# Performance work log

Hardware: AMD Instinct MI355X
Metric: run time of the kernel (lower is better)

The kernel has to match this reference:

```python
import jax, jax.numpy as jnp
import numpy as np

B, S = 32, 128
E_NUM, SKILL, D_K, D_E, D_A = 4000, 256, 128, 128, 128
AT_NUM, IT_NUM = 1000, 1000
GAMMA = 0.03


def _lin(key, out_d, in_d):
    # xavier-normal style init
    w = jax.random.normal(key, (out_d, in_d), jnp.float32) * (2.0 / (in_d + out_d)) ** 0.5
    b = jnp.zeros((out_d,), jnp.float32)
    return w, b


def setup_inputs() -> dict:
    key = jax.random.key(0)
    ks = jax.random.split(key, 16)
    exercise_id = jax.random.randint(ks[0], (B, S), 0, E_NUM, jnp.int32)
    ans_time = jax.random.randint(ks[1], (B, S), 0, AT_NUM, jnp.int32)
    interval_time = jax.random.randint(ks[2], (B, S), 0, IT_NUM, jnp.int32)
    answer_value = jax.random.randint(ks[3], (B, S), 0, 2, jnp.int32)
    # enhanced q-matrix: binary with zeros replaced by gamma
    qmask = jax.random.bernoulli(ks[4], 0.1, (E_NUM, SKILL))
    q_matrix = jnp.where(qmask, 1.0, GAMMA).astype(jnp.float32)
    ex_table = jax.random.normal(ks[5], (E_NUM, D_E), jnp.float32)
    at_table = jax.random.normal(ks[6], (AT_NUM, D_K), jnp.float32)
    it_table = jax.random.normal(ks[7], (IT_NUM, D_K), jnp.float32)
    W1, b1 = _lin(ks[8], D_K, D_E + D_K + D_A)   # learning_embed_layer
    Wl, bl = _lin(ks[9], D_K, 4 * D_K)           # learning_layer
    Wg, bg = _lin(ks[10], D_K, 4 * D_K)          # learning_gate
    Wf, bf = _lin(ks[11], D_K, 3 * D_K)          # forgetting_gate
    Wp, bp = _lin(ks[12], D_K, 2 * D_K)          # predicting_layer
    # xavier-uniform initial knowledge state, shared across batch
    lim = (6.0 / (SKILL + D_K)) ** 0.5
    h0 = jax.random.uniform(ks[13], (SKILL, D_K), jnp.float32, -lim, lim)
    return {"exercise_id": exercise_id, "ans_time": ans_time,
            "interval_time": interval_time, "answer_value": answer_value,
            "q_matrix": q_matrix, "ex_table": ex_table, "at_table": at_table,
            "it_table": it_table, "W1": W1, "b1": b1, "Wl": Wl, "bl": bl,
            "Wg": Wg, "bg": bg, "Wf": Wf, "bf": bf, "Wp": Wp, "bp": bp, "h0": h0}


def _forward(exercise_id, ans_time, interval_time, answer_value, q_matrix,
             ex_table, at_table, it_table, W1, b1, Wl, bl, Wg, bg, Wf, bf,
             Wp, bp, h0):
    b, s = exercise_id.shape
    ex = ex_table[exercise_id]                       # (B,S,d_e)
    at = at_table[ans_time]                          # (B,S,d_k)
    it = it_table[interval_time]                     # (B,S,d_k)
    ans = jnp.broadcast_to(answer_value.astype(ex.dtype)[..., None], (b, s, D_A))
    le = jnp.concatenate([ex, at, ans], -1) @ W1.T + b1   # learning embedding (B,S,d_k)
    kv = q_matrix[exercise_id]                       # knowledge vectors (B,S,skill)

    h_pre = jnp.broadcast_to(h0, (b,) + h0.shape)    # (B,skill,d_k)
    h_tilde_pre = jnp.einsum('bs,bsd->bd', kv[:, 0], h_pre)
    learning_pre = jnp.zeros((b, D_K), ex.dtype)

    def step(carry, xs):
        h_pre, h_tilde_pre, learning_pre = carry
        lv, itv, kv_t, kv_next, ex_next = xs
        x4 = jnp.concatenate([learning_pre, itv, lv, h_tilde_pre], -1)
        lg = jnp.tanh(x4 @ Wl.T + bl)
        gate = jax.nn.sigmoid(x4 @ Wg.T + bg)
        LG = gate * (lg + 1.0) * 0.5                 # (B,d_k)
        LG_tilde = kv_t[:, :, None] * LG[:, None, :] # outer product addressing (B,skill,d_k)
        x3 = jnp.concatenate([h_pre,
                              jnp.broadcast_to(LG[:, None, :], h_pre.shape),
                              jnp.broadcast_to(itv[:, None, :], h_pre.shape)], -1)
        f = jax.nn.sigmoid(x3 @ Wf.T + bf)           # forget gate per skill
        h = LG_tilde + f * h_pre                     # updated knowledge state
        h_tilde = jnp.einsum('bs,bsd->bd', kv_next, h)
        pred = jax.nn.sigmoid(jnp.concatenate([ex_next, h_tilde], -1) @ Wp.T + bp)
        return (h, h_tilde, lv), pred

    sw = lambda a: jnp.swapaxes(a, 0, 1)
    xs = (sw(le[:, :-1]), sw(it[:, 1:]), sw(kv[:, :-1]), sw(kv[:, 1:]), sw(ex[:, 1:]))
    _, preds = jax.lax.scan(step, (h_pre, h_tilde_pre, learning_pre), xs)
    return jnp.swapaxes(preds, 0, 1)                 # (B, S-1, d_k)


def reference(exercise_id, ans_time, interval_time, answer_value, q_matrix,
              ex_table, at_table, it_table, W1, b1, Wl, bl, Wg, bg, Wf, bf,
              Wp, bp, h0):
    return _forward(exercise_id, ans_time, interval_time, answer_value, q_matrix,
                    ex_table, at_table, it_table, W1, b1, Wl, bl, Wg, bg, Wf, bf,
                    Wp, bp, h0)
```

## Files before the change

### kernel.cpp

```cpp
#include <hip/hip_runtime.h>

typedef unsigned int u32;
typedef unsigned short u16;
typedef unsigned long long u64;
typedef u16 u16x8 __attribute__((ext_vector_type(8)));
typedef u16 u16x4 __attribute__((ext_vector_type(4)));
typedef __bf16 bf16x8 __attribute__((ext_vector_type(8)));
typedef __bf16 bf16x4v __attribute__((ext_vector_type(4)));
typedef float f32x4 __attribute__((ext_vector_type(4)));
typedef float f32x2 __attribute__((ext_vector_type(2)));

#define B_SZ 32
#define S_SZ 128
#define T_SZ 127
#define DK 128
#define SKILL 256
#define SQTR 64
#define RL 136
#define PP 68
#define NPAIR 8
#define SPIN_CAP (1 << 18)

__device__ __forceinline__ u16x4 cvt4(f32x4 v) {
    return __builtin_bit_cast(u16x4, __builtin_convertvector(v, bf16x4v));
}
__device__ __forceinline__ u16x8 cvt8(f32x4 a, f32x4 b) {
    u16x4 x = cvt4(a), y = cvt4(b);
    u16x8 r;
    r[0]=x[0]; r[1]=x[1]; r[2]=x[2]; r[3]=x[3];
    r[4]=y[0]; r[5]=y[1]; r[6]=y[2]; r[7]=y[3];
    return r;
}
__device__ __forceinline__ u16 bfu(float x) {
    return __builtin_bit_cast(u16, (__bf16)x);
}
__device__ __forceinline__ float sigm(float x) {
    float e = __builtin_amdgcn_exp2f(-1.44269504f * x);
    return __builtin_amdgcn_rcpf(1.f + e);
}
__device__ __forceinline__ float tanh_f(float x) {
    float e = __builtin_amdgcn_exp2f(-2.88539008f * x);
    return 2.f * __builtin_amdgcn_rcpf(1.f + e) - 1.f;
}
__device__ __forceinline__ f32x4 mfma16(u16x8 a, u16x8 bb, f32x4 c) {
    return __builtin_amdgcn_mfma_f32_16x16x32_bf16(
        __builtin_bit_cast(bf16x8, a), __builtin_bit_cast(bf16x8, bb), c, 0, 0, 0);
}
__device__ __forceinline__ float pval(u64 p) {
    return __builtin_bit_cast(float, (u32)p);
}
__device__ __forceinline__ float dot4(f32x4 w, f32x4 x) {
    return w[0] * x[0] + w[1] * x[1] + w[2] * x[2] + w[3] * x[3];
}

__global__ __launch_bounds__(128) void k_le(
    const int* __restrict__ eid, const int* __restrict__ atime,
    const int* __restrict__ ansv, const float* __restrict__ ex_t,
    const float* __restrict__ at_t, const float* __restrict__ W1,
    const float* __restrict__ b1, float* __restrict__ le_ws)
{
    const int o = threadIdx.x;
    const int p0 = blockIdx.x * NPAIR;
    int eP[NPAIR], aP[NPAIR];
    float avP[NPAIR];
    #pragma unroll
    for (int i = 0; i < NPAIR; ++i) {
        int p = p0 + i, b = p / T_SZ, t = p - b * T_SZ;
        int idx = b * S_SZ + t;
        eP[i] = eid[idx];
        aP[i] = atime[idx];
        avP[i] = (float)ansv[idx];
    }
    const float* wr = W1 + o * 384;
    const float bias = b1[o];
    float acc[NPAIR];
    #pragma unroll
    for (int i = 0; i < NPAIR; ++i) acc[i] = bias;
    #pragma unroll 2
    for (int k4 = 0; k4 < 32; ++k4) {
        f32x4 w = *(const f32x4*)(wr + 4 * k4);
        #pragma unroll
        for (int i = 0; i < NPAIR; ++i) {
            f32x4 x = *(const f32x4*)(ex_t + eP[i] * DK + 4 * k4);
            acc[i] += dot4(w, x);
        }
    }
    #pragma unroll 2
    for (int k4 = 32; k4 < 64; ++k4) {
        f32x4 w = *(const f32x4*)(wr + 4 * k4);
        #pragma unroll
        for (int i = 0; i < NPAIR; ++i) {
            f32x4 x = *(const f32x4*)(at_t + aP[i] * DK + 4 * k4 - 128);
            acc[i] += dot4(w, x);
        }
    }
    float wsum = 0.f;
    #pragma unroll 4
    for (int k4 = 64; k4 < 96; ++k4) {
        f32x4 w = *(const f32x4*)(wr + 4 * k4);
        wsum += w[0] + w[1] + w[2] + w[3];
    }
    #pragma unroll
    for (int i = 0; i < NPAIR; ++i)
        le_ws[(p0 + i) * DK + o] = acc[i] + avP[i] * wsum;
}

__global__ __launch_bounds__(128) void k_pre(
    const int* __restrict__ itime, const float* __restrict__ it_t,
    const float* __restrict__ Wl, const float* __restrict__ blv,
    const float* __restrict__ Wg, const float* __restrict__ bgv,
    const float* __restrict__ Wf, const float* __restrict__ bfv,
    const float* __restrict__ le_ws,
    float* __restrict__ PRE_l, float* __restrict__ PRE_g, float* __restrict__ PRE_f)
{
    const int o = threadIdx.x;
    const int p0 = blockIdx.x * NPAIR;
    int ivP[NPAIR], lpOff[NPAIR];
    float mP[NPAIR];
    #pragma unroll
    for (int i = 0; i < NPAIR; ++i) {
        int p = p0 + i, b = p / T_SZ, t = p - b * T_SZ;
        ivP[i] = itime[b * S_SZ + t + 1];
        mP[i] = (t == 0) ? 0.f : 1.f;
        lpOff[i] = ((t == 0) ? p : p - 1) * DK;
    }
    const float* wl = Wl + o * 512;
    const float* wg = Wg + o * 512;
    const float bl0 = blv[o], bg0 = bgv[o];
    float al[NPAIR], ag[NPAIR];
    #pragma unroll
    for (int i = 0; i < NPAIR; ++i) { al[i] = bl0; ag[i] = bg0; }
    #pragma unroll 2
    for (int k4 = 0; k4 < 32; ++k4) {
        f32x4 w  = *(const f32x4*)(wl + 4 * k4);
        f32x4 w2 = *(const f32x4*)(wg + 4 * k4);
        #pragma unroll
        for (int i = 0; i < NPAIR; ++i) {
            f32x4 x = *(const f32x4*)(le_ws + lpOff[i] + 4 * k4);
            #pragma unroll
            for (int j = 0; j < 4; ++j) {
                float xv = x[j] * mP[i];
                al[i] += w[j] * xv;
                ag[i] += w2[j] * xv;
            }
        }
    }
    #pragma unroll 2
    for (int k4 = 0; k4 < 32; ++k4) {
        f32x4 w  = *(const f32x4*)(wl + 128 + 4 * k4);
        f32x4 w2 = *(const f32x4*)(wg + 128 + 4 * k4);
        #pragma unroll
        for (int i = 0; i < NPAIR; ++i) {
            f32x4 x = *(const f32x4*)(it_t + ivP[i] * DK + 4 * k4);
            #pragma unroll
            for (int j = 0; j < 4; ++j) {
                al[i] += w[j] * x[j];
                ag[i] += w2[j] * x[j];
            }
        }
    }
    #pragma unroll 2
    for (int k4 = 0; k4 < 32; ++k4) {
        f32x4 w  = *(const f32x4*)(wl + 256 + 4 * k4);
        f32x4 w2 = *(const f32x4*)(wg + 256 + 4 * k4);
        #pragma unroll
        for (int i = 0; i < NPAIR; ++i) {
            f32x4 x = *(const f32x4*)(le_ws + (p0 + i) * DK + 4 * k4);
            #pragma unroll
            for (int j = 0; j < 4; ++j) {
                al[i] += w[j] * x[j];
                ag[i] += w2[j] * x[j];
            }
        }
    }
    const float bf0 = bfv[o];
    float af[NPAIR];
    #pragma unroll
    for (int i = 0; i < NPAIR; ++i) af[i] = bf0;
    const float* wf = Wf + o * 384 + 256;
    #pragma unroll 2
    for (int k4 = 0; k4 < 32; ++k4) {
        f32x4 w = *(const f32x4*)(wf + 4 * k4);
        #pragma unroll
        for (int i = 0; i < NPAIR; ++i) {
            f32x4 x = *(const f32x4*)(it_t + ivP[i] * DK + 4 * k4);
            af[i] += dot4(w, x);
        }
    }
    #pragma unroll
    for (int i = 0; i < NPAIR; ++i) {
        size_t idx = (size_t)(p0 + i) * DK + o;
        PRE_l[idx] = al[i];
        PRE_g[idx] = ag[i];
        PRE_f[idx] = af[i];
    }
}

__global__ __launch_bounds__(512, 1) void k_main(
    const int* __restrict__ eid, const float* __restrict__ qmat,
    const float* __restrict__ Wl, const float* __restrict__ Wg,
    const float* __restrict__ Wf, const float* __restrict__ h0,
    const float* __restrict__ PRE_l, const float* __restrict__ PRE_g,
    const float* __restrict__ PRE_f, const float* __restrict__ ex_t,
    const float* __restrict__ Wp, const float* __restrict__ bpv,
    float* __restrict__ out, u64* __restrict__ xbuf)
{
    extern __shared__ char smem[];
    u16*   hS   = (u16*)smem;
    float* part = (float*)(smem + 17408);
    u16*   htbf = (u16*)(smem + 52224);
    u16*   LGb  = (u16*)(smem + 52736);
    float* LGf  = (float*)(smem + 53248);
    float* cS   = (float*)(smem + 53760);
    float* htf  = (float*)(smem + 54272);

    const int b    = blockIdx.x;
    const int qid  = blockIdx.y;
    const int tid  = threadIdx.x;
    const int w    = tid >> 6;
    const int lane = tid & 63;
    const int quad = lane >> 4;
    const int l4   = lane & 15;
    const int ih   = w & 1;
    const int jh   = w >> 1;

    u64* xq = xbuf + (size_t)b * 1024;
    const int qa = (qid + 1) & 3, qb2 = (qid + 2) & 3, qc = (qid + 3) & 3;

    const int pj = tid >> 4;
    const int pc = tid & 15;
    f32x4 wp4[4];
    {
        const float* wpr = Wp + (32 * qid + pj) * 256 + pc * 16;
        #pragma unroll
        for (int i = 0; i < 4; ++i) wp4[i] = *(const f32x4*)(wpr + 4 * i);
    }
    const float bp = bpv[32 * qid + pj];

    u16x8 afr[4][4];
    #pragma unroll
    for (int mt = 0; mt < 4; ++mt)
        #pragma unroll
        for (int kt = 0; kt < 4; ++kt) {
            const float* p = Wf + (64 * ih + 16 * mt + l4) * 384 + 32 * kt + quad * 8;
            afr[mt][kt] = cvt8(*(const f32x4*)p, *(const f32x4*)(p + 4));
        }
    u16x8 azf[2][4];
    #pragma unroll
    for (int mt = 0; mt < 2; ++mt)
        #pragma unroll
        for (int kt = 0; kt < 4; ++kt) {
            int d = 16 * w + 8 * mt + (l4 >> 1);
            const float* base = (l4 & 1) ? Wg : Wl;
            const float* p = base + d * 512 + 384 + 32 * kt + quad * 8;
            azf[mt][kt] = cvt8(*(const f32x4*)p, *(const f32x4*)(p + 4));
        }
    u16x8 acf[4];
    #pragma unroll
    for (int kt = 0; kt < 4; ++kt) {
        const float* p = Wf + (16 * w + l4) * 384 + 128 + 32 * kt + quad * 8;
        acf[kt] = cvt8(*(const f32x4*)p, *(const f32x4*)(p + 4));
    }

    const int sl = 16 * jh + l4;
    f32x4 hreg[4];
    #pragma unroll
    for (int mt = 0; mt < 4; ++mt) {
        int d0 = 64 * ih + 16 * mt + quad * 4;
        f32x4 hv = *(const f32x4*)(h0 + (SQTR * qid + sl) * DK + d0);
        hreg[mt] = hv;
        *(u16x4*)(hS + sl * RL + d0) = cvt4(hv);
    }

    float kvt = qmat[eid[b * S_SZ] * SKILL + SQTR * qid + sl];

    f32x4 accF[4];

    {
        float htp[16];
        #pragma unroll
        for (int mt = 0; mt < 4; ++mt)
            #pragma unroll
            for (int r = 0; r < 4; ++r)
                htp[mt * 4 + r] = kvt * hreg[mt][r];
        #pragma unroll
        for (int mt = 0; mt < 4; ++mt)
            #pragma unroll
            for (int r = 0; r < 4; ++r)
                part[(64 * ih + 16 * mt + quad * 4 + r) * PP + jh * 16 + l4] = htp[mt * 4 + r];
        __syncthreads();
        int d = tid >> 2, kq = tid & 3;
        const float* pp = part + d * PP + kq * 16;
        float v = 0.f;
        #pragma unroll
        for (int i4 = 0; i4 < 4; ++i4) {
            f32x4 x = *(const f32x4*)(pp + 4 * i4);
            v += x[0] + x[1] + x[2] + x[3];
        }
        v += __shfl_xor(v, 1, 64);
        v += __shfl_xor(v, 2, 64);
        if (kq == 0) {
            u64 pkt = ((u64)1u << 32) | (u64)__builtin_bit_cast(u32, v);
            __hip_atomic_store(xq + qid * 256 + 128 + d, pkt,
                               __ATOMIC_RELAXED, __HIP_MEMORY_SCOPE_AGENT);
        }
        asm volatile("" ::: "memory");
        #pragma unroll
        for (int mt = 0; mt < 4; ++mt)
            accF[mt] = (f32x4){0.f, 0.f, 0.f, 0.f};
        {
            const u16* bp2 = hS + sl * RL + quad * 8;
            u16x8 bfr[4];
            #pragma unroll
            for (int kt = 0; kt < 4; ++kt) bfr[kt] = *(const u16x8*)(bp2 + kt * 32);
            #pragma unroll
            for (int mt = 0; mt < 4; ++mt)
                #pragma unroll
                for (int kt = 0; kt < 4; ++kt)
                    accF[mt] = mfma16(afr[mt][kt], bfr[kt], accF[mt]);
        }
        if (kq == 0) {
            u64 pa, pb, pc2;
            int spins = 0;
            do {
                pa  = __hip_atomic_load(xq + qa * 256 + 128 + d, __ATOMIC_RELAXED, __HIP_MEMORY_SCOPE_AGENT);
                pb  = __hip_atomic_load(xq + qb2 * 256 + 128 + d, __ATOMIC_RELAXED, __HIP_MEMORY_SCOPE_AGENT);
                pc2 = __hip_atomic_load(xq + qc * 256 + 128 + d, __ATOMIC_RELAXED, __HIP_MEMORY_SCOPE_AGENT);
                if ((u32)(pa >> 32) >= 1u && (u32)(pb >> 32) >= 1u && (u32)(pc2 >> 32) >= 1u) break;
                if (spins > 64) __builtin_amdgcn_s_sleep(1);
            } while (++spins < SPIN_CAP);
            float va = pval(pa), vb = pval(pb), vc = pval(pc2);
            float v0 = (qid == 0) ? v : (qid == 3) ? va : (qid == 2) ? vb : vc;
            float v1 = (qid == 1) ? v : (qid == 0) ? va : (qid == 3) ? vb : vc;
            float v2 = (qid == 2) ? v : (qid == 1) ? va : (qid == 0) ? vb : vc;
            float v3 = (qid == 3) ? v : (qid == 2) ? va : (qid == 1) ? vb : vc;
            float vt = ((v0 + v1) + v2) + v3;
            float hf = (float)(__bf16)vt;
            htbf[d] = bfu(vt);
            htbf[128 + d] = bfu(vt - hf);
        }
        __syncthreads();
    }

    for (int t = 0; t < T_SZ; ++t) {
        const size_t tb = (size_t)(b * T_SZ + t) * DK;

        if (t > 0) {
            int epid = eid[b * S_SZ + t];
            float pacc;
            if (pc < 8) {
                const float* xr = ex_t + epid * DK + pc * 16;
                pacc  = dot4(wp4[0], *(const f32x4*)xr);
                pacc += dot4(wp4[1], *(const f32x4*)(xr + 4));
                pacc += dot4(wp4[2], *(const f32x4*)(xr + 8));
                pacc += dot4(wp4[3], *(const f32x4*)(xr + 12));
            } else {
                const float* xr = htf + (pc - 8) * 16;
                pacc  = dot4(wp4[0], *(const f32x4*)xr);
                pacc += dot4(wp4[1], *(const f32x4*)(xr + 4));
                pacc += dot4(wp4[2], *(const f32x4*)(xr + 8));
                pacc += dot4(wp4[3], *(const f32x4*)(xr + 12));
            }
            pacc += __shfl_xor(pacc, 1, 64);
            pacc += __shfl_xor(pacc, 2, 64);
            pacc += __shfl_xor(pacc, 4, 64);
            pacc += __shfl_xor(pacc, 8, 64);
            if (pc == 0)
                out[(size_t)(b * T_SZ + t - 1) * DK + 32 * qid + pj] = sigm(pacc + bp);
        }

        float kvn = qmat[eid[b * S_SZ + t + 1] * SKILL + SQTR * qid + sl];
        f32x2 pl[2], pg[2];
        #pragma unroll
        for (int mt = 0; mt < 2; ++mt) {
            int d0 = 16 * w + 8 * mt + 2 * quad;
            pl[mt] = *(const f32x2*)(PRE_l + tb + d0);
            pg[mt] = *(const f32x2*)(PRE_g + tb + d0);
        }
        f32x4 pf = *(const f32x4*)(PRE_f + tb + 16 * w + quad * 4);

        f32x4 accZ[2];
        accZ[0] = (f32x4){0.f, 0.f, 0.f, 0.f};
        accZ[1] = (f32x4){0.f, 0.f, 0.f, 0.f};
        #pragma unroll
        for (int kt = 0; kt < 4; ++kt) {
            u16x8 bh = *(const u16x8*)(htbf + 32 * kt + quad * 8);
            u16x8 bl = *(const u16x8*)(htbf + 128 + 32 * kt + quad * 8);
            #pragma unroll
            for (int mt = 0; mt < 2; ++mt) {
                accZ[mt] = mfma16(azf[mt][kt], bh, accZ[mt]);
                accZ[mt] = mfma16(azf[mt][kt], bl, accZ[mt]);
            }
        }
        #pragma unroll
        for (int mt = 0; mt < 2; ++mt) {
            u32 hpack = 0, lpack = 0;
            f32x2 fpack;
            #pragma unroll
            for (int rp = 0; rp < 2; ++rp) {
                float zl = accZ[mt][2 * rp] + pl[mt][rp];
                float zg = accZ[mt][2 * rp + 1] + pg[mt][rp];
                float LGv = sigm(zg) * (tanh_f(zl) + 1.f) * 0.5f;
                float hif = (float)(__bf16)LGv;
                hpack |= ((u32)bfu(LGv)) << (16 * rp);
                lpack |= ((u32)bfu(LGv - hif)) << (16 * rp);
                fpack[rp] = LGv;
            }
            if (l4 == 0) {
                int d0 = 16 * w + 8 * mt + 2 * quad;
                *(u32*)(LGb + d0) = hpack;
                *(u32*)(LGb + 128 + d0) = lpack;
                *(f32x2*)(LGf + d0) = fpack;
            }
        }
        __syncthreads();

        {
            f32x4 accC = (f32x4){0.f, 0.f, 0.f, 0.f};
            #pragma unroll
            for (int kt = 0; kt < 4; ++kt) {
                u16x8 bh = *(const u16x8*)(LGb + 32 * kt + quad * 8);
                u16x8 bl = *(const u16x8*)(LGb + 128 + 32 * kt + quad * 8);
                accC = mfma16(acf[kt], bh, accC);
                accC = mfma16(acf[kt], bl, accC);
            }
            accC += pf;
            if (l4 == 0) *(f32x4*)(cS + 16 * w + quad * 4) = accC;
        }
        __syncthreads();

        float htp[16];
        #pragma unroll
        for (int mt = 0; mt < 4; ++mt) {
            int d0 = 64 * ih + 16 * mt + quad * 4;
            f32x4 lg = *(const f32x4*)(LGf + d0);
            f32x4 cc = *(const f32x4*)(cS + d0);
            f32x4 hv;
            #pragma unroll
            for (int r = 0; r < 4; ++r) {
                float f = sigm(accF[mt][r] + cc[r]);
                float hn = kvt * lg[r] + f * hreg[mt][r];
                hreg[mt][r] = hn;
                htp[mt * 4 + r] = kvn * hn;
                hv[r] = hn;
            }
            *(u16x4*)(hS + sl * RL + d0) = cvt4(hv);
        }
        #pragma unroll
        for (int mt = 0; mt < 4; ++mt)
            #pragma unroll
            for (int r = 0; r < 4; ++r)
                part[(64 * ih + 16 * mt + quad * 4 + r) * PP + jh * 16 + l4] = htp[mt * 4 + r];
        kvt = kvn;
        __syncthreads();

        {
            int d = tid >> 2, kq = tid & 3;
            const float* pp = part + d * PP + kq * 16;
            float v = 0.f;
            #pragma unroll
            for (int i4 = 0; i4 < 4; ++i4) {
                f32x4 x = *(const f32x4*)(pp + 4 * i4);
                v += x[0] + x[1] + x[2] + x[3];
            }
            v += __shfl_xor(v, 1, 64);
            v += __shfl_xor(v, 2, 64);
            const int slot = t & 1;
            const u32 seq = (u32)(t + 2);
            if (kq == 0) {
                u64 pkt = ((u64)seq << 32) | (u64)__builtin_bit_cast(u32, v);
                __hip_atomic_store(xq + qid * 256 + slot * 128 + d, pkt,
                                   __ATOMIC_RELAXED, __HIP_MEMORY_SCOPE_AGENT);
            }
            asm volatile("" ::: "memory");
            #pragma unroll
            for (int mt = 0; mt < 4; ++mt)
                accF[mt] = (f32x4){0.f, 0.f, 0.f, 0.f};
            {
                const u16* bp2 = hS + sl * RL + quad * 8;
                u16x8 bfr[4];
                #pragma unroll
                for (int kt = 0; kt < 4; ++kt) bfr[kt] = *(const u16x8*)(bp2 + kt * 32);
                #pragma unroll
                for (int mt = 0; mt < 4; ++mt)
                    #pragma unroll
                    for (int kt = 0; kt < 4; ++kt)
                        accF[mt] = mfma16(afr[mt][kt], bfr[kt], accF[mt]);
            }
            if (kq == 0) {
                u64 pa, pb, pc2;
                int spins = 0;
                do {
                    pa  = __hip_atomic_load(xq + qa * 256 + slot * 128 + d, __ATOMIC_RELAXED, __HIP_MEMORY_SCOPE_AGENT);
                    pb  = __hip_atomic_load(xq + qb2 * 256 + slot * 128 + d, __ATOMIC_RELAXED, __HIP_MEMORY_SCOPE_AGENT);
                    pc2 = __hip_atomic_load(xq + qc * 256 + slot * 128 + d, __ATOMIC_RELAXED, __HIP_MEMORY_SCOPE_AGENT);
                    if ((u32)(pa >> 32) >= seq && (u32)(pb >> 32) >= seq && (u32)(pc2 >> 32) >= seq) break;
                    if (spins > 64) __builtin_amdgcn_s_sleep(1);
                } while (++spins < SPIN_CAP);
                float va = pval(pa), vb = pval(pb), vc = pval(pc2);
                float v0 = (qid == 0) ? v : (qid == 3) ? va : (qid == 2) ? vb : vc;
                float v1 = (qid == 1) ? v : (qid == 0) ? va : (qid == 3) ? vb : vc;
                float v2 = (qid == 2) ? v : (qid == 1) ? va : (qid == 0) ? vb : vc;
                float v3 = (qid == 3) ? v : (qid == 2) ? va : (qid == 1) ? vb : vc;
                float vt = ((v0 + v1) + v2) + v3;
                float hf = (float)(__bf16)vt;
                htbf[d] = bfu(vt);
                htbf[128 + d] = bfu(vt - hf);
                htf[d] = vt;
            }
        }
        __syncthreads();
    }

    {
        int epid = eid[b * S_SZ + T_SZ];
        float pacc;
        if (pc < 8) {
            const float* xr = ex_t + epid * DK + pc * 16;
            pacc  = dot4(wp4[0], *(const f32x4*)xr);
            pacc += dot4(wp4[1], *(const f32x4*)(xr + 4));
            pacc += dot4(wp4[2], *(const f32x4*)(xr + 8));
            pacc += dot4(wp4[3], *(const f32x4*)(xr + 12));
        } else {
            const float* xr = htf + (pc - 8) * 16;
            pacc  = dot4(wp4[0], *(const f32x4*)xr);
            pacc += dot4(wp4[1], *(const f32x4*)(xr + 4));
            pacc += dot4(wp4[2], *(const f32x4*)(xr + 8));
            pacc += dot4(wp4[3], *(const f32x4*)(xr + 12));
        }
        pacc += __shfl_xor(pacc, 1, 64);
        pacc += __shfl_xor(pacc, 2, 64);
        pacc += __shfl_xor(pacc, 4, 64);
        pacc += __shfl_xor(pacc, 8, 64);
        if (pc == 0)
            out[(size_t)(b * T_SZ + T_SZ - 1) * DK + 32 * qid + pj] = sigm(pacc + bp);
    }
}

extern "C" void kernel_launch(void* const* d_in, const int* in_sizes, int n_in,
                              void* d_out, int out_size, void* d_ws, size_t ws_size,
                              hipStream_t stream) {
    const int* eid     = (const int*)d_in[0];
    const int* atime   = (const int*)d_in[1];
    const int* itime   = (const int*)d_in[2];
    const int* ansv    = (const int*)d_in[3];
    const float* qmat  = (const float*)d_in[4];
    const float* ex_t  = (const float*)d_in[5];
    const float* at_t  = (const float*)d_in[6];
    const float* it_t  = (const float*)d_in[7];
    const float* W1    = (const float*)d_in[8];
    const float* b1    = (const float*)d_in[9];
    const float* Wl    = (const float*)d_in[10];
    const float* blv   = (const float*)d_in[11];
    const float* Wg    = (const float*)d_in[12];
    const float* bgv   = (const float*)d_in[13];
    const float* Wf    = (const float*)d_in[14];
    const float* bfv   = (const float*)d_in[15];
    const float* Wp    = (const float*)d_in[16];
    const float* bpv   = (const float*)d_in[17];
    const float* h0    = (const float*)d_in[18];
    float* out = (float*)d_out;

    const size_t SZ = (size_t)B_SZ * T_SZ * DK;
    float* wsf   = (float*)d_ws;
    float* le_ws = wsf;
    float* PRE_l = wsf + SZ;
    float* PRE_g = wsf + 2 * SZ;
    float* PRE_f = wsf + 3 * SZ;
    u64* xbuf = (u64*)le_ws;

    hipFuncSetAttribute((const void*)k_main,
                        hipFuncAttributeMaxDynamicSharedMemorySize, 86016);

    dim3 gaux(508);
    k_le  <<<gaux, 128, 0, stream>>>(eid, atime, ansv, ex_t, at_t, W1, b1, le_ws);
    k_pre <<<gaux, 128, 0, stream>>>(itime, it_t, Wl, blv, Wg, bgv, Wf, bfv,
                                     le_ws, PRE_l, PRE_g, PRE_f);
    hipMemsetAsync(xbuf, 0, (size_t)B_SZ * 1024 * sizeof(u64), stream);
    k_main<<<dim3(B_SZ, 4), 512, 86016, stream>>>(eid, qmat, Wl, Wg, Wf, h0,
                                                  PRE_l, PRE_g, PRE_f,
                                                  ex_t, Wp, bpv, out, xbuf);
}
```

Measured before the change: 662.9 us.

## Fuse precompute and prediction into one persistent kernel with producer-consumer flags

Merges the learning-embed and gate precompute kernels into a single kernel with extra roles (blockIdx.y 4 and 5). The helper blocks compute PRE_l/PRE_g/PRE_f in time chunks and publish per-chunk flags, and the recurrent blocks consume them as they become ready. The output prediction projection moves off the recurrent critical path into helper blocks that read a journal of h_tilde values. The aim is to overlap the precompute with the serial scan, drop separate launches, and shorten per-step recurrent work. The cost is spin-wait synchronisation between co-resident blocks, which depends on all 192 blocks being resident at once and risks stalls or deadlock otherwise.

```diff
diff --git a/kernel.cpp b/kernel.cpp
--- a/kernel.cpp
+++ b/kernel.cpp
@@ -18,7 +18,8 @@
 #define SQTR 64
 #define RL 136
 #define PP 68
-#define NPAIR 8
+#define SLOTS 4
+#define SLOTM 3
 #define SPIN_CAP (1 << 18)
 
 __device__ __forceinline__ u16x4 cvt4(f32x4 v) {
@@ -52,409 +53,108 @@
 __device__ __forceinline__ float dot4(f32x4 w, f32x4 x) {
     return w[0] * x[0] + w[1] * x[1] + w[2] * x[2] + w[3] * x[3];
 }
-
-__global__ __launch_bounds__(128) void k_le(
+__device__ __forceinline__ float aldf(const float* p) {
+    return __hip_atomic_load(p, __ATOMIC_RELAXED, __HIP_MEMORY_SCOPE_AGENT);
+}
+__device__ __forceinline__ void astf(float* p, float v) {
+    __hip_atomic_store(p, v, __ATOMIC_RELAXED, __HIP_MEMORY_SCOPE_AGENT);
+}
+__device__ __forceinline__ u64 ald64(const u64* p) {
+    return __hip_atomic_load(p, __ATOMIC_RELAXED, __HIP_MEMORY_SCOPE_AGENT);
+}
+__device__ __forceinline__ void ast64(u64* p, u64 v) {
+    __hip_atomic_store(p, v, __ATOMIC_RELAXED, __HIP_MEMORY_SCOPE_AGENT);
+}
+
+__global__ __launch_bounds__(512, 1) void k_mono(
     const int* __restrict__ eid, const int* __restrict__ atime,
-    const int* __restrict__ ansv, const float* __restrict__ ex_t,
-    const float* __restrict__ at_t, const float* __restrict__ W1,
-    const float* __restrict__ b1, float* __restrict__ le_ws)
-{
-    const int o = threadIdx.x;
-    const int p0 = blockIdx.x * NPAIR;
-    int eP[NPAIR], aP[NPAIR];
-    float avP[NPAIR];
-    #pragma unroll
-    for (int i = 0; i < NPAIR; ++i) {
-        int p = p0 + i, b = p / T_SZ, t = p - b * T_SZ;
-        int idx = b * S_SZ + t;
-        eP[i] = eid[idx];
-        aP[i] = atime[idx];
-        avP[i] = (float)ansv[idx];
-    }
-    const float* wr = W1 + o * 384;
-    const float bias = b1[o];
-    float acc[NPAIR];
-    #pragma unroll
-    for (int i = 0; i < NPAIR; ++i) acc[i] = bias;
-    #pragma unroll 2
-    for (int k4 = 0; k4 < 32; ++k4) {
-        f32x4 w = *(const f32x4*)(wr + 4 * k4);
-        #pragma unroll
-        for (int i = 0; i < NPAIR; ++i) {
-            f32x4 x = *(const f32x4*)(ex_t + eP[i] * DK + 4 * k4);
-            acc[i] += dot4(w, x);
-        }
-    }
-    #pragma unroll 2
-    for (int k4 = 32; k4 < 64; ++k4) {
-        f32x4 w = *(const f32x4*)(wr + 4 * k4);
-        #pragma unroll
-        for (int i = 0; i < NPAIR; ++i) {
-            f32x4 x = *(const f32x4*)(at_t + aP[i] * DK + 4 * k4 - 128);
-            acc[i] += dot4(w, x);
-        }
-    }
-    float wsum = 0.f;
-    #pragma unroll 4
-    for (int k4 = 64; k4 < 96; ++k4) {
-        f32x4 w = *(const f32x4*)(wr + 4 * k4);
-        wsum += w[0] + w[1] + w[2] + w[3];
-    }
-    #pragma unroll
-    for (int i = 0; i < NPAIR; ++i)
-        le_ws[(p0 + i) * DK + o] = acc[i] + avP[i] * wsum;
-}
-
-__global__ __launch_bounds__(128) void k_pre(
-    const int* __restrict__ itime, const float* __restrict__ it_t,
+    const int* __restrict__ itime, const int* __restrict__ ansv,
+    const float* __restrict__ qmat, const float* __restrict__ ex_t,
+    const float* __restrict__ at_t, const float* __restrict__ it_t,
+    const float* __restrict__ W1, const float* __restrict__ b1,
     const float* __restrict__ Wl, const float* __restrict__ blv,
     const float* __restrict__ Wg, const float* __restrict__ bgv,
     const float* __restrict__ Wf, const float* __restrict__ bfv,
-    const float* __restrict__ le_ws,
-    float* __restrict__ PRE_l, float* __restrict__ PRE_g, float* __restrict__ PRE_f)
-{
-    const int o = threadIdx.x;
-    const int p0 = blockIdx.x * NPAIR;
-    int ivP[NPAIR], lpOff[NPAIR];
-    float mP[NPAIR];
-    #pragma unroll
-    for (int i = 0; i < NPAIR; ++i) {
-        int p = p0 + i, b = p / T_SZ, t = p - b * T_SZ;
-        ivP[i] = itime[b * S_SZ + t + 1];
-        mP[i] = (t == 0) ? 0.f : 1.f;
-        lpOff[i] = ((t == 0) ? p : p - 1) * DK;
-    }
-    const float* wl = Wl + o * 512;
-    const float* wg = Wg + o * 512;
-    const float bl0 = blv[o], bg0 = bgv[o];
-    float al[NPAIR], ag[NPAIR];
-    #pragma unroll
-    for (int i = 0; i < NPAIR; ++i) { al[i] = bl0; ag[i] = bg0; }
-    #pragma unroll 2
-    for (int k4 = 0; k4 < 32; ++k4) {
-        f32x4 w  = *(const f32x4*)(wl + 4 * k4);
-        f32x4 w2 = *(const f32x4*)(wg + 4 * k4);
-        #pragma unroll
-        for (int i = 0; i < NPAIR; ++i) {
-            f32x4 x = *(const f32x4*)(le_ws + lpOff[i] + 4 * k4);
-            #pragma unroll
-            for (int j = 0; j < 4; ++j) {
-                float xv = x[j] * mP[i];
-                al[i] += w[j] * xv;
-                ag[i] += w2[j] * xv;
-            }
-        }
-    }
-    #pragma unroll 2
-    for (int k4 = 0; k4 < 32; ++k4) {
-        f32x4 w  = *(const f32x4*)(wl + 128 + 4 * k4);
-        f32x4 w2 = *(const f32x4*)(wg + 128 + 4 * k4);
-        #pragma unroll
-        for (int i = 0; i < NPAIR; ++i) {
-            f32x4 x = *(const f32x4*)(it_t + ivP[i] * DK + 4 * k4);
-            #pragma unroll
-            for (int j = 0; j < 4; ++j) {
-                al[i] += w[j] * x[j];
-                ag[i] += w2[j] * x[j];
-            }
-        }
-    }
-    #pragma unroll 2
-    for (int k4 = 0; k4 < 32; ++k4) {
-        f32x4 w  = *(const f32x4*)(wl + 256 + 4 * k4);
-        f32x4 w2 = *(const f32x4*)(wg + 256 + 4 * k4);
-        #pragma unroll
-        for (int i = 0; i < NPAIR; ++i) {
-            f32x4 x = *(const f32x4*)(le_ws + (p0 + i) * DK + 4 * k4);
-            #pragma unroll
-            for (int j = 0; j < 4; ++j) {
-                al[i] += w[j] * x[j];
-                ag[i] += w2[j] * x[j];
-            }
-        }
-    }
-    const float bf0 = bfv[o];
-    float af[NPAIR];
-    #pragma unroll
-    for (int i = 0; i < NPAIR; ++i) af[i] = bf0;
-    const float* wf = Wf + o * 384 + 256;
-    #pragma unroll 2
-    for (int k4 = 0; k4 < 32; ++k4) {
-        f32x4 w = *(const f32x4*)(wf + 4 * k4);
-        #pragma unroll
-        for (int i = 0; i < NPAIR; ++i) {
-            f32x4 x = *(const f32x4*)(it_t + ivP[i] * DK + 4 * k4);
-            af[i] += dot4(w, x);
-        }
-    }
-    #pragma unroll
-    for (int i = 0; i < NPAIR; ++i) {
-        size_t idx = (size_t)(p0 + i) * DK + o;
-        PRE_l[idx] = al[i];
-        PRE_g[idx] = ag[i];
-        PRE_f[idx] = af[i];
-    }
-}
-
-__global__ __launch_bounds__(512, 1) void k_main(
-    const int* __restrict__ eid, const float* __restrict__ qmat,
-    const float* __restrict__ Wl, const float* __restrict__ Wg,
-    const float* __restrict__ Wf, const float* __restrict__ h0,
-    const float* __restrict__ PRE_l, const float* __restrict__ PRE_g,
-    const float* __restrict__ PRE_f, const float* __restrict__ ex_t,
     const float* __restrict__ Wp, const float* __restrict__ bpv,
-    float* __restrict__ out, u64* __restrict__ xbuf)
+    const float* __restrict__ h0,
+    float* __restrict__ PRE_l, float* __restrict__ PRE_g, float* __restrict__ PRE_f,
+    float* __restrict__ out, u64* __restrict__ xbuf, float* __restrict__ jrnF,
+    int* __restrict__ jflg, int* __restrict__ flagsP)
 {
     extern __shared__ char smem[];
-    u16*   hS   = (u16*)smem;
-    float* part = (float*)(smem + 17408);
-    u16*   htbf = (u16*)(smem + 52224);
-    u16*   LGb  = (u16*)(smem + 52736);
-    float* LGf  = (float*)(smem + 53248);
-    float* cS   = (float*)(smem + 53760);
-    float* htf  = (float*)(smem + 54272);
-
     const int b    = blockIdx.x;
-    const int qid  = blockIdx.y;
+    const int role = blockIdx.y;
     const int tid  = threadIdx.x;
-    const int w    = tid >> 6;
-    const int lane = tid & 63;
-    const int quad = lane >> 4;
-    const int l4   = lane & 15;
-    const int ih   = w & 1;
-    const int jh   = w >> 1;
-
-    u64* xq = xbuf + (size_t)b * 1024;
-    const int qa = (qid + 1) & 3, qb2 = (qid + 2) & 3, qc = (qid + 3) & 3;
-
-    const int pj = tid >> 4;
-    const int pc = tid & 15;
-    f32x4 wp4[4];
-    {
-        const float* wpr = Wp + (32 * qid + pj) * 256 + pc * 16;
+    u64* xq = xbuf + (size_t)b * (4 * SLOTS * 128);
+
+    if (role < 4) {
+        u16*   hS   = (u16*)smem;
+        float* part = (float*)(smem + 17408);
+        u16*   htbf = (u16*)(smem + 52224);
+        u16*   LGb  = (u16*)(smem + 52736);
+        float* LGf  = (float*)(smem + 53248);
+        float* cS   = (float*)(smem + 53760);
+
+        const int qid  = role;
+        const int w    = tid >> 6;
+        const int lane = tid & 63;
+        const int quad = lane >> 4;
+        const int l4   = lane & 15;
+        const int ih   = w & 1;
+        const int jh   = w >> 1;
+        const int qa = (qid + 1) & 3, qb2 = (qid + 2) & 3, qc = (qid + 3) & 3;
+
+        u16x8 afr[4][4];
         #pragma unroll
-        for (int i = 0; i < 4; ++i) wp4[i] = *(const f32x4*)(wpr + 4 * i);
-    }
-    const float bp = bpv[32 * qid + pj];
-
-    u16x8 afr[4][4];
-    #pragma unroll
-    for (int mt = 0; mt < 4; ++mt)
+        for (int mt = 0; mt < 4; ++mt)
+            #pragma unroll
+            for (int kt = 0; kt < 4; ++kt) {
+                const float* p = Wf + (64 * ih + 16 * mt + l4) * 384 + 32 * kt + quad * 8;
+                afr[mt][kt] = cvt8(*(const f32x4*)p, *(const f32x4*)(p + 4));
+            }
+        u16x8 azf[2][4];
+        #pragma unroll
+        for (int mt = 0; mt < 2; ++mt)
+            #pragma unroll
+            for (int kt = 0; kt < 4; ++kt) {
+                int d = 16 * w + 8 * mt + (l4 >> 1);
+                const float* base = (l4 & 1) ? Wg : Wl;
+                const float* p = base + d * 512 + 384 + 32 * kt + quad * 8;
+                azf[mt][kt] = cvt8(*(const f32x4*)p, *(const f32x4*)(p + 4));
+            }
+        u16x8 acf[4];
         #pragma unroll
         for (int kt = 0; kt < 4; ++kt) {
-            const float* p = Wf + (64 * ih + 16 * mt + l4) * 384 + 32 * kt + quad * 8;
-            afr[mt][kt] = cvt8(*(const f32x4*)p, *(const f32x4*)(p + 4));
-        }
-    u16x8 azf[2][4];
-    #pragma unroll
-    for (int mt = 0; mt < 2; ++mt)
-        #pragma unroll
-        for (int kt = 0; kt < 4; ++kt) {
-            int d = 16 * w + 8 * mt + (l4 >> 1);
-            const float* base = (l4 & 1) ? Wg : Wl;
-            const float* p = base + d * 512 + 384 + 32 * kt + quad * 8;
-            azf[mt][kt] = cvt8(*(const f32x4*)p, *(const f32x4*)(p + 4));
-        }
-    u16x8 acf[4];
-    #pragma unroll
-    for (int kt = 0; kt < 4; ++kt) {
-        const float* p = Wf + (16 * w + l4) * 384 + 128 + 32 * kt + quad * 8;
-        acf[kt] = cvt8(*(const f32x4*)p, *(const f32x4*)(p + 4));
-    }
-
-    const int sl = 16 * jh + l4;
-    f32x4 hreg[4];
-    #pragma unroll
-    for (int mt = 0; mt < 4; ++mt) {
-        int d0 = 64 * ih + 16 * mt + quad * 4;
-        f32x4 hv = *(const f32x4*)(h0 + (SQTR * qid + sl) * DK + d0);
-        hreg[mt] = hv;
-        *(u16x4*)(hS + sl * RL + d0) = cvt4(hv);
-    }
-
-    float kvt = qmat[eid[b * S_SZ] * SKILL + SQTR * qid + sl];
-
-    f32x4 accF[4];
-
-    {
-        float htp[16];
-        #pragma unroll
-        for (int mt = 0; mt < 4; ++mt)
-            #pragma unroll
-            for (int r = 0; r < 4; ++r)
-                htp[mt * 4 + r] = kvt * hreg[mt][r];
-        #pragma unroll
-        for (int mt = 0; mt < 4; ++mt)
-            #pragma unroll
-            for (int r = 0; r < 4; ++r)
-                part[(64 * ih + 16 * mt + quad * 4 + r) * PP + jh * 16 + l4] = htp[mt * 4 + r];
-        __syncthreads();
-        int d = tid >> 2, kq = tid & 3;
-        const float* pp = part + d * PP + kq * 16;
-        float v = 0.f;
-        #pragma unroll
-        for (int i4 = 0; i4 < 4; ++i4) {
-            f32x4 x = *(const f32x4*)(pp + 4 * i4);
-            v += x[0] + x[1] + x[2] + x[3];
-        }
-        v += __shfl_xor(v, 1, 64);
-        v += __shfl_xor(v, 2, 64);
-        if (kq == 0) {
-            u64 pkt = ((u64)1u << 32) | (u64)__builtin_bit_cast(u32, v);
-            __hip_atomic_store(xq + qid * 256 + 128 + d, pkt,
-                               __ATOMIC_RELAXED, __HIP_MEMORY_SCOPE_AGENT);
-        }
-        asm volatile("" ::: "memory");
-        #pragma unroll
-        for (int mt = 0; mt < 4; ++mt)
-            accF[mt] = (f32x4){0.f, 0.f, 0.f, 0.f};
-        {
-            const u16* bp2 = hS + sl * RL + quad * 8;
-            u16x8 bfr[4];
-            #pragma unroll
-            for (int kt = 0; kt < 4; ++kt) bfr[kt] = *(const u16x8*)(bp2 + kt * 32);
-            #pragma unroll
-            for (int mt = 0; mt < 4; ++mt)
-                #pragma unroll
-                for (int kt = 0; kt < 4; ++kt)
-                    accF[mt] = mfma16(afr[mt][kt], bfr[kt], accF[mt]);
-        }
-        if (kq == 0) {
-            u64 pa, pb, pc2;
-            int spins = 0;
-            do {
-                pa  = __hip_atomic_load(xq + qa * 256 + 128 + d, __ATOMIC_RELAXED, __HIP_MEMORY_SCOPE_AGENT);
-                pb  = __hip_atomic_load(xq + qb2 * 256 + 128 + d, __ATOMIC_RELAXED, __HIP_MEMORY_SCOPE_AGENT);
-                pc2 = __hip_atomic_load(xq + qc * 256 + 128 + d, __ATOMIC_RELAXED, __HIP_MEMORY_SCOPE_AGENT);
-                if ((u32)(pa >> 32) >= 1u && (u32)(pb >> 32) >= 1u && (u32)(pc2 >> 32) >= 1u) break;
-                if (spins > 64) __builtin_amdgcn_s_sleep(1);
-            } while (++spins < SPIN_CAP);
-            float va = pval(pa), vb = pval(pb), vc = pval(pc2);
-            float v0 = (qid == 0) ? v : (qid == 3) ? va : (qid == 2) ? vb : vc;
-            float v1 = (qid == 1) ? v : (qid == 0) ? va : (qid == 3) ? vb : vc;
-            float v2 = (qid == 2) ? v : (qid == 1) ? va : (qid == 0) ? vb : vc;
-            float v3 = (qid == 3) ? v : (qid == 2) ? va : (qid == 1) ? vb : vc;
-            float vt = ((v0 + v1) + v2) + v3;
-            float hf = (float)(__bf16)vt;
-            htbf[d] = bfu(vt);
-            htbf[128 + d] = bfu(vt - hf);
-        }
-        __syncthreads();
-    }
-
-    for (int t = 0; t < T_SZ; ++t) {
-        const size_t tb = (size_t)(b * T_SZ + t) * DK;
-
-        if (t > 0) {
-            int epid = eid[b * S_SZ + t];
-            float pacc;
-            if (pc < 8) {
-                const float* xr = ex_t + epid * DK + pc * 16;
-                pacc  = dot4(wp4[0], *(const f32x4*)xr);
-                pacc += dot4(wp4[1], *(const f32x4*)(xr + 4));
-                pacc += dot4(wp4[2], *(const f32x4*)(xr + 8));
-                pacc += dot4(wp4[3], *(const f32x4*)(xr + 12));
-            } else {
-                const float* xr = htf + (pc - 8) * 16;
-                pacc  = dot4(wp4[0], *(const f32x4*)xr);
-                pacc += dot4(wp4[1], *(const f32x4*)(xr + 4));
-                pacc += dot4(wp4[2], *(const f32x4*)(xr + 8));
-                pacc += dot4(wp4[3], *(const f32x4*)(xr + 12));
-            }
-            pacc += __shfl_xor(pacc, 1, 64);
-            pacc += __shfl_xor(pacc, 2, 64);
-            pacc += __shfl_xor(pacc, 4, 64);
-            pacc += __shfl_xor(pacc, 8, 64);
-            if (pc == 0)
-                out[(size_t)(b * T_SZ + t - 1) * DK + 32 * qid + pj] = sigm(pacc + bp);
-        }
-
-        float kvn = qmat[eid[b * S_SZ + t + 1] * SKILL + SQTR * qid + sl];
-        f32x2 pl[2], pg[2];
-        #pragma unroll
-        for (int mt = 0; mt < 2; ++mt) {
-            int d0 = 16 * w + 8 * mt + 2 * quad;
-            pl[mt] = *(const f32x2*)(PRE_l + tb + d0);
-            pg[mt] = *(const f32x2*)(PRE_g + tb + d0);
-        }
-        f32x4 pf = *(const f32x4*)(PRE_f + tb + 16 * w + quad * 4);
-
-        f32x4 accZ[2];
-        accZ[0] = (f32x4){0.f, 0.f, 0.f, 0.f};
-        accZ[1] = (f32x4){0.f, 0.f, 0.f, 0.f};
-        #pragma unroll
-        for (int kt = 0; kt < 4; ++kt) {
-            u16x8 bh = *(const u16x8*)(htbf + 32 * kt + quad * 8);
-            u16x8 bl = *(const u16x8*)(htbf + 128 + 32 * kt + quad * 8);
-            #pragma unroll
-            for (int mt = 0; mt < 2; ++mt) {
-                accZ[mt] = mfma16(azf[mt][kt], bh, accZ[mt]);
-                accZ[mt] = mfma16(azf[mt][kt], bl, accZ[mt]);
-            }
-        }
-        #pragma unroll
-        for (int mt = 0; mt < 2; ++mt) {
-            u32 hpack = 0, lpack = 0;
-            f32x2 fpack;
-            #pragma unroll
-            for (int rp = 0; rp < 2; ++rp) {
-                float zl = accZ[mt][2 * rp] + pl[mt][rp];
-                float zg = accZ[mt][2 * rp + 1] + pg[mt][rp];
-                float LGv = sigm(zg) * (tanh_f(zl) + 1.f) * 0.5f;
-                float hif = (float)(__bf16)LGv;
-                hpack |= ((u32)bfu(LGv)) << (16 * rp);
-                lpack |= ((u32)bfu(LGv - hif)) << (16 * rp);
-                fpack[rp] = LGv;
-            }
-            if (l4 == 0) {
-                int d0 = 16 * w + 8 * mt + 2 * quad;
-                *(u32*)(LGb + d0) = hpack;
-                *(u32*)(LGb + 128 + d0) = lpack;
-                *(f32x2*)(LGf + d0) = fpack;
-            }
-        }
-        __syncthreads();
-
-        {
-            f32x4 accC = (f32x4){0.f, 0.f, 0.f, 0.f};
-            #pragma unroll
-            for (int kt = 0; kt < 4; ++kt) {
-                u16x8 bh = *(const u16x8*)(LGb + 32 * kt + quad * 8);
-                u16x8 bl = *(const u16x8*)(LGb + 128 + 32 * kt + quad * 8);
-                accC = mfma16(acf[kt], bh, accC);
-                accC = mfma16(acf[kt], bl, accC);
-            }
-            accC += pf;
-            if (l4 == 0) *(f32x4*)(cS + 16 * w + quad * 4) = accC;
-        }
-        __syncthreads();
-
-        float htp[16];
+            const float* p = Wf + (16 * w + l4) * 384 + 128 + 32 * kt + quad * 8;
+            acf[kt] = cvt8(*(const f32x4*)p, *(const f32x4*)(p + 4));
+        }
+
+        const int sl = 16 * jh + l4;
+        f32x4 hreg[4];
         #pragma unroll
         for (int mt = 0; mt < 4; ++mt) {
             int d0 = 64 * ih + 16 * mt + quad * 4;
-            f32x4 lg = *(const f32x4*)(LGf + d0);
-            f32x4 cc = *(const f32x4*)(cS + d0);
-            f32x4 hv;
-            #pragma unroll
-            for (int r = 0; r < 4; ++r) {
-                float f = sigm(accF[mt][r] + cc[r]);
-                float hn = kvt * lg[r] + f * hreg[mt][r];
-                hreg[mt][r] = hn;
-                htp[mt * 4 + r] = kvn * hn;
-                hv[r] = hn;
-            }
+            f32x4 hv = *(const f32x4*)(h0 + (SQTR * qid + sl) * DK + d0);
+            hreg[mt] = hv;
             *(u16x4*)(hS + sl * RL + d0) = cvt4(hv);
         }
-        #pragma unroll
-        for (int mt = 0; mt < 4; ++mt)
-            #pragma unroll
-            for (int r = 0; r < 4; ++r)
-                part[(64 * ih + 16 * mt + quad * 4 + r) * PP + jh * 16 + l4] = htp[mt * 4 + r];
-        kvt = kvn;
-        __syncthreads();
+
+        float kvt = qmat[eid[b * S_SZ] * SKILL + SQTR * qid + sl];
+        f32x4 accF[4];
 
         {
+            float htp[16];
+            #pragma unroll
+            for (int mt = 0; mt < 4; ++mt)
+                #pragma unroll
+                for (int r = 0; r < 4; ++r)
+                    htp[mt * 4 + r] = kvt * hreg[mt][r];
+            #pragma unroll
+            for (int mt = 0; mt < 4; ++mt)
+                #pragma unroll
+                for (int r = 0; r < 4; ++r)
+                    part[(64 * ih + 16 * mt + quad * 4 + r) * PP + jh * 16 + l4] = htp[mt * 4 + r];
+            __syncthreads();
             int d = tid >> 2, kq = tid & 3;
             const float* pp = part + d * PP + kq * 16;
             float v = 0.f;
@@ -465,13 +165,9 @@
             }
             v += __shfl_xor(v, 1, 64);
             v += __shfl_xor(v, 2, 64);
-            const int slot = t & 1;
-            const u32 seq = (u32)(t + 2);
-            if (kq == 0) {
-                u64 pkt = ((u64)seq << 32) | (u64)__builtin_bit_cast(u32, v);
-                __hip_atomic_store(xq + qid * 256 + slot * 128 + d, pkt,
-                                   __ATOMIC_RELAXED, __HIP_MEMORY_SCOPE_AGENT);
-            }
+            if (kq == 0)
+                ast64(xq + qid * (SLOTS * 128) + 1 * 128 + d,
+                      ((u64)1u << 32) | (u64)__builtin_bit_cast(u32, v));
             asm volatile("" ::: "memory");
             #pragma unroll
             for (int mt = 0; mt < 4; ++mt)
@@ -491,10 +187,10 @@
                 u64 pa, pb, pc2;
                 int spins = 0;
                 do {
-                    pa  = __hip_atomic_load(xq + qa * 256 + slot * 128 + d, __ATOMIC_RELAXED, __HIP_MEMORY_SCOPE_AGENT);
-                    pb  = __hip_atomic_load(xq + qb2 * 256 + slot * 128 + d, __ATOMIC_RELAXED, __HIP_MEMORY_SCOPE_AGENT);
-                    pc2 = __hip_atomic_load(xq + qc * 256 + slot * 128 + d, __ATOMIC_RELAXED, __HIP_MEMORY_SCOPE_AGENT);
-                    if ((u32)(pa >> 32) >= seq && (u32)(pb >> 32) >= seq && (u32)(pc2 >> 32) >= seq) break;
+                    pa  = ald64(xq + qa  * (SLOTS * 128) + 128 + d);
+                    pb  = ald64(xq + qb2 * (SLOTS * 128) + 128 + d);
+                    pc2 = ald64(xq + qc  * (SLOTS * 128) + 128 + d);
+                    if ((u32)(pa >> 32) >= 1u && (u32)(pb >> 32) >= 1u && (u32)(pc2 >> 32) >= 1u) break;
                     if (spins > 64) __builtin_amdgcn_s_sleep(1);
                 } while (++spins < SPIN_CAP);
                 float va = pval(pa), vb = pval(pb), vc = pval(pc2);
@@ -506,34 +202,331 @@
                 float hf = (float)(__bf16)vt;
                 htbf[d] = bfu(vt);
                 htbf[128 + d] = bfu(vt - hf);
-                htf[d] = vt;
+            }
+            __syncthreads();
+        }
+
+        for (int t = 0; t < T_SZ; ++t) {
+            const size_t tb = (size_t)(b * T_SZ + t) * DK;
+
+            if ((t & 3) == 0) {
+                const int gI = t >> 2;
+                int spins = 0;
+                while (__hip_atomic_load(flagsP + b * 32 + gI,
+                                         __ATOMIC_RELAXED, __HIP_MEMORY_SCOPE_AGENT) == 0) {
+                    if (spins > 16) __builtin_amdgcn_s_sleep(1);
+                    if (++spins > SPIN_CAP) break;
+                }
+            }
+
+            float kvn = qmat[eid[b * S_SZ + t + 1] * SKILL + SQTR * qid + sl];
+            float plv[2][2], pgv[2][2], pfv[4];
+            #pragma unroll
+            for (int mt = 0; mt < 2; ++mt) {
+                int d0 = 16 * w + 8 * mt + 2 * quad;
+                plv[mt][0] = aldf(PRE_l + tb + d0);
+                plv[mt][1] = aldf(PRE_l + tb + d0 + 1);
+                pgv[mt][0] = aldf(PRE_g + tb + d0);
+                pgv[mt][1] = aldf(PRE_g + tb + d0 + 1);
+            }
+            #pragma unroll
+            for (int r = 0; r < 4; ++r)
+                pfv[r] = aldf(PRE_f + tb + 16 * w + 4 * quad + r);
+
+            f32x4 accZ[2];
+            accZ[0] = (f32x4){0.f, 0.f, 0.f, 0.f};
+            accZ[1] = (f32x4){0.f, 0.f, 0.f, 0.f};
+            #pragma unroll
+            for (int kt = 0; kt < 4; ++kt) {
+                u16x8 bh = *(const u16x8*)(htbf + 32 * kt + quad * 8);
+                u16x8 bl = *(const u16x8*)(htbf + 128 + 32 * kt + quad * 8);
+                #pragma unroll
+                for (int mt = 0; mt < 2; ++mt) {
+                    accZ[mt] = mfma16(azf[mt][kt], bh, accZ[mt]);
+                    accZ[mt] = mfma16(azf[mt][kt], bl, accZ[mt]);
+                }
+            }
+            #pragma unroll
+            for (int mt = 0; mt < 2; ++mt) {
+                u32 hpack = 0, lpack = 0;
+                f32x2 fpack;
+                #pragma unroll
+                for (int rp = 0; rp < 2; ++rp) {
+                    float zl = accZ[mt][2 * rp] + plv[mt][rp];
+                    float zg = accZ[mt][2 * rp + 1] + pgv[mt][rp];
+                    float LGv = sigm(zg) * (tanh_f(zl) + 1.f) * 0.5f;
+                    float hif = (float)(__bf16)LGv;
+                    hpack |= ((u32)bfu(LGv)) << (16 * rp);
+                    lpack |= ((u32)bfu(LGv - hif)) << (16 * rp);
+                    fpack[rp] = LGv;
+                }
+                if (l4 == 0) {
+                    int d0 = 16 * w + 8 * mt + 2 * quad;
+                    *(u32*)(LGb + d0) = hpack;
+                    *(u32*)(LGb + 128 + d0) = lpack;
+                    *(f32x2*)(LGf + d0) = fpack;
+                }
+            }
+            __syncthreads();
+
+            {
+                f32x4 accC = (f32x4){0.f, 0.f, 0.f, 0.f};
+                #pragma unroll
+                for (int kt = 0; kt < 4; ++kt) {
+                    u16x8 bh = *(const u16x8*)(LGb + 32 * kt + quad * 8);
+                    u16x8 bl = *(const u16x8*)(LGb + 128 + 32 * kt + quad * 8);
+                    accC = mfma16(acf[kt], bh, accC);
+                    accC = mfma16(acf[kt], bl, accC);
+                }
+                #pragma unroll
+                for (int r = 0; r < 4; ++r) accC[r] += pfv[r];
+                if (l4 == 0) *(f32x4*)(cS + 16 * w + quad * 4) = accC;
+            }
+            __syncthreads();
+
+            float htp[16];
+            #pragma unroll
+            for (int mt = 0; mt < 4; ++mt) {
+                int d0 = 64 * ih + 16 * mt + quad * 4;
+                f32x4 lg = *(const f32x4*)(LGf + d0);
+                f32x4 cc = *(const f32x4*)(cS + d0);
+                f32x4 hv;
+                #pragma unroll
+                for (int r = 0; r < 4; ++r) {
+                    float f = sigm(accF[mt][r] + cc[r]);
+                    float hn = kvt * lg[r] + f * hreg[mt][r];
+                    hreg[mt][r] = hn;
+                    htp[mt * 4 + r] = kvn * hn;
+                    hv[r] = hn;
+                }
+                *(u16x4*)(hS + sl * RL + d0) = cvt4(hv);
+            }
+            #pragma unroll
+            for (int mt = 0; mt < 4; ++mt)
+                #pragma unroll
+                for (int r = 0; r < 4; ++r)
+                    part[(64 * ih + 16 * mt + quad * 4 + r) * PP + jh * 16 + l4] = htp[mt * 4 + r];
+            kvt = kvn;
+            __syncthreads();
+
+            {
+                int d = tid >> 2, kq = tid & 3;
+                const float* pp = part + d * PP + kq * 16;
+                float v = 0.f;
+                #pragma unroll
+                for (int i4 = 0; i4 < 4; ++i4) {
+                    f32x4 x = *(const f32x4*)(pp + 4 * i4);
+                    v += x[0] + x[1] + x[2] + x[3];
+                }
+                v += __shfl_xor(v, 1, 64);
+                v += __shfl_xor(v, 2, 64);
+                const u32 seq = (u32)(t + 2);
+                const int slot = (int)(seq & SLOTM);
+                if (kq == 0)
+                    ast64(xq + qid * (SLOTS * 128) + slot * 128 + d,
+                          ((u64)seq << 32) | (u64)__builtin_bit_cast(u32, v));
+                asm volatile("" ::: "memory");
+                #pragma unroll
+                for (int mt = 0; mt < 4; ++mt)
+                    accF[mt] = (f32x4){0.f, 0.f, 0.f, 0.f};
+                {
+                    const u16* bp2 = hS + sl * RL + quad * 8;
+                    u16x8 bfr[4];
+                    #pragma unroll
+                    for (int kt = 0; kt < 4; ++kt) bfr[kt] = *(const u16x8*)(bp2 + kt * 32);
+                    #pragma unroll
+                    for (int mt = 0; mt < 4; ++mt)
+                        #pragma unroll
+                        for (int kt = 0; kt < 4; ++kt)
+                            accF[mt] = mfma16(afr[mt][kt], bfr[kt], accF[mt]);
+                }
+                if (kq == 0) {
+                    u64 pa, pb, pc2;
+                    int spins = 0;
+                    do {
+                        pa  = ald64(xq + qa  * (SLOTS * 128) + slot * 128 + d);
+                        pb  = ald64(xq + qb2 * (SLOTS * 128) + slot * 128 + d);
+                        pc2 = ald64(xq + qc  * (SLOTS * 128) + slot * 128 + d);
+                        if ((u32)(pa >> 32) >= seq && (u32)(pb >> 32) >= seq && (u32)(pc2 >> 32) >= seq) break;
+                        if (spins > 64) __builtin_amdgcn_s_sleep(1);
+                    } while (++spins < SPIN_CAP);
+                    float va = pval(pa), vb = pval(pb), vc = pval(pc2);
+                    float v0 = (qid == 0) ? v : (qid == 3) ? va : (qid == 2) ? vb : vc;
+                    float v1 = (qid == 1) ? v : (qid == 0) ? va : (qid == 3) ? vb : vc;
+                    float v2 = (qid == 2) ? v : (qid == 1) ? va : (qid == 0) ? vb : vc;
+                    float v3 = (qid == 3) ? v : (qid == 2) ? va : (qid == 1) ? vb : vc;
+                    float vt = ((v0 + v1) + v2) + v3;
+                    float hf = (float)(__bf16)vt;
+                    htbf[d] = bfu(vt);
+                    htbf[128 + d] = bfu(vt - hf);
+                    if (qid == 0)
+                        astf(jrnF + ((size_t)b * T_SZ + t) * 128 + d, vt);
+                }
+            }
+            if (qid == 0) asm volatile("s_waitcnt vmcnt(0)" ::: "memory");
+            __syncthreads();
+            if (qid == 0 && tid == 0)
+                __hip_atomic_store(jflg + b * T_SZ + t, 1,
+                                   __ATOMIC_RELAXED, __HIP_MEMORY_SCOPE_AGENT);
+        }
+    } else {
+        const int p  = role - 4;
+        const int o  = tid & 127;
+        const int g  = tid >> 7;
+        const int t0 = 64 * p;
+        const int tend = (t0 + 64 < T_SZ) ? t0 + 64 : T_SZ;
+        float* leP   = (float*)smem;
+        float* htP   = (float*)(smem + 33280);
+        float* part2 = (float*)(smem + 33792);
+
+        const float* w1r = W1 + o * 384;
+        const float b1o = b1[o];
+        float wsum = 0.f;
+        #pragma unroll 4
+        for (int k4 = 64; k4 < 96; ++k4) {
+            f32x4 w = *(const f32x4*)(w1r + 4 * k4);
+            wsum += w[0] + w[1] + w[2] + w[3];
+        }
+        if (g == 0) {
+            if (t0 == 0) {
+                leP[o] = 0.f;
+            } else {
+                int tt = t0 - 1, idx = b * S_SZ + tt;
+                int e = eid[idx], a = atime[idx];
+                float av = (float)ansv[idx];
+                float acc = b1o;
+                #pragma unroll 2
+                for (int k4 = 0; k4 < 32; ++k4)
+                    acc += dot4(*(const f32x4*)(w1r + 4 * k4),
+                                *(const f32x4*)(ex_t + e * DK + 4 * k4));
+                #pragma unroll 2
+                for (int k4 = 32; k4 < 64; ++k4)
+                    acc += dot4(*(const f32x4*)(w1r + 4 * k4),
+                                *(const f32x4*)(at_t + a * DK + 4 * k4 - 128));
+                leP[o] = acc + av * wsum;
             }
         }
         __syncthreads();
-    }
-
-    {
-        int epid = eid[b * S_SZ + T_SZ];
-        float pacc;
-        if (pc < 8) {
-            const float* xr = ex_t + epid * DK + pc * 16;
-            pacc  = dot4(wp4[0], *(const f32x4*)xr);
-            pacc += dot4(wp4[1], *(const f32x4*)(xr + 4));
-            pacc += dot4(wp4[2], *(const f32x4*)(xr + 8));
-            pacc += dot4(wp4[3], *(const f32x4*)(xr + 12));
-        } else {
-            const float* xr = htf + (pc - 8) * 16;
-            pacc  = dot4(wp4[0], *(const f32x4*)xr);
-            pacc += dot4(wp4[1], *(const f32x4*)(xr + 4));
-            pacc += dot4(wp4[2], *(const f32x4*)(xr + 8));
-            pacc += dot4(wp4[3], *(const f32x4*)(xr + 12));
-        }
-        pacc += __shfl_xor(pacc, 1, 64);
-        pacc += __shfl_xor(pacc, 2, 64);
-        pacc += __shfl_xor(pacc, 4, 64);
-        pacc += __shfl_xor(pacc, 8, 64);
-        if (pc == 0)
-            out[(size_t)(b * T_SZ + T_SZ - 1) * DK + 32 * qid + pj] = sigm(pacc + bp);
+
+        const float* wl = Wl + o * 512;
+        const float* wg = Wg + o * 512;
+        const float* wf = Wf + o * 384 + 256;
+        const float bl0 = blv[o], bg0 = bgv[o], bf0 = bfv[o];
+
+        for (int gi2 = 0; gi2 < 16; ++gi2) {
+            int tg = t0 + 4 * gi2;
+            if (tg >= tend) break;
+            int t = tg + g;
+            bool act = (t < tend);
+            if (act) {
+                int idx = b * S_SZ + t;
+                int e = eid[idx], a = atime[idx];
+                float av = (float)ansv[idx];
+                float acc = b1o;
+                #pragma unroll 2
+                for (int k4 = 0; k4 < 32; ++k4)
+                    acc += dot4(*(const f32x4*)(w1r + 4 * k4),
+                                *(const f32x4*)(ex_t + e * DK + 4 * k4));
+                #pragma unroll 2
+                for (int k4 = 32; k4 < 64; ++k4)
+                    acc += dot4(*(const f32x4*)(w1r + 4 * k4),
+                                *(const f32x4*)(at_t + a * DK + 4 * k4 - 128));
+                leP[(t - t0 + 1) * 128 + o] = acc + av * wsum;
+            }
+            __syncthreads();
+            if (act) {
+                const float* lp = leP + (t - t0) * 128;
+                const float* lc = leP + (t - t0 + 1) * 128;
+                const float mP = (t == 0) ? 0.f : 1.f;
+                int iv = itime[b * S_SZ + t + 1];
+                float al = bl0, ag = bg0;
+                #pragma unroll 2
+                for (int k4 = 0; k4 < 32; ++k4) {
+                    f32x4 w  = *(const f32x4*)(wl + 4 * k4);
+                    f32x4 w2 = *(const f32x4*)(wg + 4 * k4);
+                    f32x4 x  = *(const f32x4*)(lp + 4 * k4);
+                    #pragma unroll
+                    for (int j = 0; j < 4; ++j) {
+                        float xv = x[j] * mP;
+                        al += w[j] * xv; ag += w2[j] * xv;
+                    }
+                }
+                #pragma unroll 2
+                for (int k4 = 0; k4 < 32; ++k4) {
+                    f32x4 w  = *(const f32x4*)(wl + 128 + 4 * k4);
+                    f32x4 w2 = *(const f32x4*)(wg + 128 + 4 * k4);
+                    f32x4 x  = *(const f32x4*)(it_t + iv * DK + 4 * k4);
+                    #pragma unroll
+                    for (int j = 0; j < 4; ++j) {
+                        al += w[j] * x[j]; ag += w2[j] * x[j];
+                    }
+                }
+                #pragma unroll 2
+                for (int k4 = 0; k4 < 32; ++k4) {
+                    f32x4 w  = *(const f32x4*)(wl + 256 + 4 * k4);
+                    f32x4 w2 = *(const f32x4*)(wg + 256 + 4 * k4);
+                    f32x4 x  = *(const f32x4*)(lc + 4 * k4);
+                    #pragma unroll
+                    for (int j = 0; j < 4; ++j) {
+                        al += w[j] * x[j]; ag += w2[j] * x[j];
+                    }
+                }
+                float af = bf0;
+                #pragma unroll 2
+                for (int k4 = 0; k4 < 32; ++k4)
+                    af += dot4(*(const f32x4*)(wf + 4 * k4),
+                               *(const f32x4*)(it_t + iv * DK + 4 * k4));
+                size_t idx2 = (size_t)(b * T_SZ + t) * DK + o;
+                astf(PRE_l + idx2, al);
+                astf(PRE_g + idx2, ag);
+                astf(PRE_f + idx2, af);
+            }
+            asm volatile("s_waitcnt vmcnt(0)" ::: "memory");
+            __syncthreads();
+            if (tid == 0)
+                __hip_atomic_store(flagsP + b * 32 + (tg >> 2), 1,
+                                   __ATOMIC_RELAXED, __HIP_MEMORY_SCOPE_AGENT);
+        }
+
+        f32x4 wp[16];
+        {
+            const float* wpr = Wp + o * 256 + 64 * g;
+            #pragma unroll
+            for (int i = 0; i < 16; ++i) wp[i] = *(const f32x4*)(wpr + 4 * i);
+        }
+        const float bp_o = bpv[o];
+        for (int t = t0; t < tend; ++t) {
+            if (g == 0) {
+                int sp = 0;
+                while (__hip_atomic_load(jflg + b * T_SZ + t,
+                                         __ATOMIC_RELAXED, __HIP_MEMORY_SCOPE_AGENT) == 0) {
+                    if (sp > 64) __builtin_amdgcn_s_sleep(1);
+                    if (++sp > SPIN_CAP) break;
+                }
+                htP[o] = aldf(jrnF + ((size_t)b * T_SZ + t) * 128 + o);
+            }
+            __syncthreads();
+            int e2 = eid[b * S_SZ + t + 1];
+            float acc = 0.f;
+            if (g < 2) {
+                const float* xr = ex_t + e2 * DK + 64 * g;
+                #pragma unroll 4
+                for (int k = 0; k < 16; ++k)
+                    acc += dot4(wp[k], *(const f32x4*)(xr + 4 * k));
+            } else {
+                const float* xr = htP + 64 * (g - 2);
+                #pragma unroll 4
+                for (int k = 0; k < 16; ++k)
+                    acc += dot4(wp[k], *(const f32x4*)(xr + 4 * k));
+            }
+            part2[g * 128 + o] = acc;
+            __syncthreads();
+            if (g == 0) {
+                float s = ((part2[o] + part2[128 + o]) + part2[256 + o]) + part2[384 + o] + bp_o;
+                out[(size_t)(b * T_SZ + t) * DK + o] = sigm(s);
+            }
+            __syncthreads();
+        }
     }
 }
 
@@ -563,21 +556,20 @@
 
     const size_t SZ = (size_t)B_SZ * T_SZ * DK;
     float* wsf   = (float*)d_ws;
-    float* le_ws = wsf;
+    u64* xbuf   = (u64*)wsf;
+    int* flagsP = (int*)(xbuf + 32 * 16 * 128);
+    int* jflg   = flagsP + 32 * 32;
     float* PRE_l = wsf + SZ;
     float* PRE_g = wsf + 2 * SZ;
     float* PRE_f = wsf + 3 * SZ;
-    u64* xbuf = (u64*)le_ws;
-
-    hipFuncSetAttribute((const void*)k_main,
+    float* jrnF  = wsf + 4 * SZ;
+
+    hipFuncSetAttribute((const void*)k_mono,
                         hipFuncAttributeMaxDynamicSharedMemorySize, 86016);
 
-    dim3 gaux(508);
-    k_le  <<<gaux, 128, 0, stream>>>(eid, atime, ansv, ex_t, at_t, W1, b1, le_ws);
-    k_pre <<<gaux, 128, 0, stream>>>(itime, it_t, Wl, blv, Wg, bgv, Wf, bfv,
-                                     le_ws, PRE_l, PRE_g, PRE_f);
-    hipMemsetAsync(xbuf, 0, (size_t)B_SZ * 1024 * sizeof(u64), stream);
-    k_main<<<dim3(B_SZ, 4), 512, 86016, stream>>>(eid, qmat, Wl, Wg, Wf, h0,
-                                                  PRE_l, PRE_g, PRE_f,
-                                                  ex_t, Wp, bpv, out, xbuf);
-}
+    hipMemsetAsync(wsf, 0, 524288 + 32 * 32 * 4 + 32 * T_SZ * 4, stream);
+    k_mono<<<dim3(B_SZ, 6), 512, 86016, stream>>>(
+        eid, atime, itime, ansv, qmat, ex_t, at_t, it_t, W1, b1,
+        Wl, blv, Wg, bgv, Wf, bfv, Wp, bpv, h0,
+        PRE_l, PRE_g, PRE_f, out, xbuf, jrnF, jflg, flagsP);
+}
```

After: 1.560 ms. 135% more time.
